# Performance work log

Measured on AMD Instinct MI355X. Metric: run time of the kernel, lower is better.

## Reference

```python
import jax, jax.numpy as jnp
import numpy as np

T, S, B, D, H, DH, DI = 1024, 1024, 4, 1024, 16, 64, 4096
SCALE = 1.0 / (DH ** 0.5)


def _ln(x, g, b, eps=1e-5):
    m = jnp.mean(x, axis=-1, keepdims=True)
    v = jnp.mean((x - m) ** 2, axis=-1, keepdims=True)
    return (x - m) * jax.lax.rsqrt(v + eps) * g + b


def setup_inputs() -> dict:
    key = jax.random.key(0)
    ks = jax.random.split(key, 16)
    s = 0.02
    inp = {
        "dec_inp": jax.random.normal(ks[0], (T, B, D), jnp.float32),
        "enc_out": jax.random.normal(ks[1], (T, B, D), jnp.float32),
        # causal mask for self-attn: [qlen, klen, bsz], True = masked
        "dec_mask": jnp.broadcast_to(jnp.triu(jnp.ones((T, T), bool), 1)[:, :, None], (T, T, B)),
        # encoder padding mask: [klen, bsz], last 128 positions padded
        "enc_mask": jnp.broadcast_to((jnp.arange(S) >= S - 128)[:, None], (S, B)),
        # self-attn params
        "W_q1": jax.random.normal(ks[2], (D, H * DH), jnp.float32) * s,
        "W_kv1": jax.random.normal(ks[3], (D, 2 * H * DH), jnp.float32) * s,
        "W_o1": jax.random.normal(ks[4], (H * DH, D), jnp.float32) * s,
        "g1": jnp.ones((D,), jnp.float32), "b1": jnp.zeros((D,), jnp.float32),
        # cross-attn params
        "W_q2": jax.random.normal(ks[5], (D, H * DH), jnp.float32) * s,
        "W_kv2": jax.random.normal(ks[6], (D, 2 * H * DH), jnp.float32) * s,
        "W_o2": jax.random.normal(ks[7], (H * DH, D), jnp.float32) * s,
        "g2": jnp.ones((D,), jnp.float32), "b2": jnp.zeros((D,), jnp.float32),
        # FFN params
        "W_ff1": jax.random.normal(ks[8], (D, DI), jnp.float32) * s,
        "b_ff1": jnp.zeros((DI,), jnp.float32),
        "W_ff2": jax.random.normal(ks[9], (DI, D), jnp.float32) * s,
        "b_ff2": jnp.zeros((D,), jnp.float32),
        "g3": jnp.ones((D,), jnp.float32), "b3": jnp.zeros((D,), jnp.float32),
    }
    return inp


def reference(dec_inp, enc_out, dec_mask, enc_mask,
              W_q1, W_kv1, W_o1, g1, b1,
              W_q2, W_kv2, W_o2, g2, b2,
              W_ff1, b_ff1, W_ff2, b_ff2, g3, b3):
    # ---- self-attention (MultiHeadAttn, pre_lnorm=True, mems=None) ----
    # NOTE: q is computed from the UN-normalized h; k,v from LN(c) — faithful to source.
    c = _ln(dec_inp, g1, b1)
    q = (dec_inp @ W_q1).reshape(T, B, H, DH)
    kv = (c @ W_kv1)
    k, v = jnp.split(kv, 2, axis=-1)
    k = k.reshape(T, B, H, DH)
    v = v.reshape(T, B, H, DH)
    score = jnp.einsum('ibnd,jbnd->ijbn', q, k) * SCALE  # [T,T,B,H]
    score = jnp.where(dec_mask[:, :, :, None], -jnp.inf, score)
    prob = jax.nn.softmax(score, axis=1)
    vec = jnp.einsum('ijbn,jbnd->ibnd', prob, v).reshape(T, B, H * DH)
    out1 = dec_inp + vec @ W_o1

    # ---- cross-attention (ContextMultiHeadAttn, pre_lnorm=True) ----
    # NOTE: residual uses the layer-normed h (source reassigns h = layer_norm(h)).
    h2 = _ln(out1, g2, b2)
    q2 = (h2 @ W_q2).reshape(T, B, H, DH)
    kv2 = enc_out @ W_kv2  # enc_out is NOT layer-normed in source
    k2, v2 = jnp.split(kv2, 2, axis=-1)
    k2 = k2.reshape(S, B, H, DH)
    v2 = v2.reshape(S, B, H, DH)
    score2 = jnp.einsum('ibnd,jbnd->ijbn', q2, k2) * SCALE  # [T,S,B,H]
    score2 = jnp.where(enc_mask[None, :, :, None], -10000.0, score2)
    prob2 = jax.nn.softmax(score2, axis=1)
    vec2 = jnp.einsum('ijbn,jbnd->ibnd', prob2, v2).reshape(T, B, H * DH)
    out2 = h2 + vec2 @ W_o2

    # ---- position-wise FFN (pre_lnorm) ----
    h3 = _ln(out2, g3, b3)
    core = jax.nn.gelu(h3 @ W_ff1 + b_ff1, approximate=False) @ W_ff2 + b_ff2
    return out2 + core
```

## Files before the change

kernel.cpp:

```cpp
#include <hip/hip_runtime.h>
#include <hip/hip_bf16.h>

#define T_ 1024
#define S_ 1024
#define B_ 4
#define D_ 1024
#define H_ 16
#define DH_ 64
#define DI_ 4096
#define NTOK 4096

typedef __attribute__((ext_vector_type(8))) short bf16x8;
typedef __attribute__((ext_vector_type(4))) float f32x4;

__device__ __forceinline__ short f2bf(float f) {
  unsigned u = __builtin_bit_cast(unsigned, f);
  u += 0x7fffu + ((u >> 16) & 1u);
  return (short)(u >> 16);
}

__device__ __forceinline__ void g2l16(const void* g, void* l) {
  __builtin_amdgcn_global_load_lds(
      (const __attribute__((address_space(1))) unsigned int*)g,
      (__attribute__((address_space(3))) unsigned int*)l, 16, 0, 0);
}

__device__ __forceinline__ void bar() {
  asm volatile("" ::: "memory");
  __builtin_amdgcn_s_barrier();
  asm volatile("" ::: "memory");
}

template <int EPI>
__global__ __launch_bounds__(512, 2) void gemm8p(
    const short* __restrict__ A, const short* __restrict__ Bt,
    float* __restrict__ outF, short* __restrict__ outB,
    const float* __restrict__ res, const float* __restrict__ bias,
    int M, int N, int K) {
  __shared__ short sA[2][256 * 64];
  __shared__ short sB[2][256 * 64];
  const int tid = threadIdx.x;
  const int lane = tid & 63;
  const int w = tid >> 6;
  const int wm = w >> 2, wn = w & 3;
  const int r15 = lane & 15, g4 = lane >> 4;
  const size_t row0 = (size_t)blockIdx.x * 256;
  const size_t col0 = (size_t)blockIdx.y * 256;

  f32x4 acc[8][4];
#pragma unroll
  for (int i = 0; i < 8; i++)
#pragma unroll
    for (int j = 0; j < 4; j++) acc[i][j] = (f32x4){0.f, 0.f, 0.f, 0.f};

  auto stageA = [&](int buf, int s, int kt) {
    const int k0 = kt << 6;
#pragma unroll
    for (int j = 0; j < 2; ++j) {
      const int c = j * 8 + w;
      const int rb = ((c >> 3) << 7) + (s << 6) + ((c & 7) << 3);
      const int row = rb + (lane >> 3);
      const int col = k0 + (((lane & 7) ^ (row & 7)) << 3);
      g2l16(A + (row0 + row) * (size_t)K + col, &sA[buf][rb * 64]);
    }
  };
  auto stageB = [&](int buf, int s, int kt) {
    const int k0 = kt << 6;
#pragma unroll
    for (int j = 0; j < 2; ++j) {
      const int c = j * 8 + w;
      const int rb = ((c >> 2) << 6) + (s << 5) + ((c & 3) << 3);
      const int row = rb + (lane >> 3);
      const int col = k0 + (((lane & 7) ^ (row & 7)) << 3);
      g2l16(Bt + (col0 + row) * (size_t)K + col, &sB[buf][rb * 64]);
    }
  };

  const int nk = K >> 6;
  stageA(0, 0, 0); stageA(0, 1, 0); stageB(0, 0, 0); stageB(0, 1, 0);
  if (nk > 1) {
    stageA(1, 0, 1); stageB(1, 1, 1);
    asm volatile("s_waitcnt vmcnt(4)" ::: "memory");
  } else {
    asm volatile("s_waitcnt vmcnt(0)" ::: "memory");
  }
  bar();

  bf16x8 af[4][2], bv0[2][2], bv1[2][2];
  for (int t = 0; t < nk; ++t) {
    const int cur = t & 1;
    const short* cA = sA[cur];
    const short* cB = sB[cur];
#pragma unroll
    for (int mi = 0; mi < 4; mi++) {
      const int rowA = wm * 128 + mi * 16 + r15;
#pragma unroll
      for (int kk = 0; kk < 2; kk++)
        af[mi][kk] = *(const bf16x8*)(cA + rowA * 64 +
                                      (((kk * 4 + g4) ^ (rowA & 7)) << 3));
    }
#pragma unroll
    for (int ni = 0; ni < 2; ni++) {
      const int rowB = wn * 64 + ni * 16 + r15;
#pragma unroll
      for (int kk = 0; kk < 2; kk++)
        bv0[ni][kk] = *(const bf16x8*)(cB + rowB * 64 +
                                       (((kk * 4 + g4) ^ (rowB & 7)) << 3));
    }
    if (t + 1 < nk) stageA(cur ^ 1, 1, t + 1);
    bar();
    asm volatile("s_waitcnt lgkmcnt(0)" ::: "memory");
    __builtin_amdgcn_s_setprio(1);
#pragma unroll
    for (int kk = 0; kk < 2; kk++)
#pragma unroll
      for (int mi = 0; mi < 4; mi++)
#pragma unroll
        for (int ni = 0; ni < 2; ni++)
          acc[mi][ni] = __builtin_amdgcn_mfma_f32_16x16x32_bf16(
              af[mi][kk], bv0[ni][kk], acc[mi][ni], 0, 0, 0);
    __builtin_amdgcn_s_setprio(0);
    bar();
#pragma unroll
    for (int ni = 0; ni < 2; ni++) {
      const int rowB = wn * 64 + (2 + ni) * 16 + r15;
#pragma unroll
      for (int kk = 0; kk < 2; kk++)
        bv1[ni][kk] = *(const bf16x8*)(cB + rowB * 64 +
                                       (((kk * 4 + g4) ^ (rowB & 7)) << 3));
    }
    if (t + 1 < nk) stageB(cur ^ 1, 0, t + 1);
    bar();
    asm volatile("s_waitcnt lgkmcnt(0)" ::: "memory");
    __builtin_amdgcn_s_setprio(1);
#pragma unroll
    for (int kk = 0; kk < 2; kk++)
#pragma unroll
      for (int mi = 0; mi < 4; mi++)
#pragma unroll
        for (int ni = 0; ni < 2; ni++)
          acc[mi][2 + ni] = __builtin_amdgcn_mfma_f32_16x16x32_bf16(
              af[mi][kk], bv1[ni][kk], acc[mi][2 + ni], 0, 0, 0);
    __builtin_amdgcn_s_setprio(0);
    bar();
#pragma unroll
    for (int mi = 0; mi < 4; mi++) {
      const int rowA = wm * 128 + (4 + mi) * 16 + r15;
#pragma unroll
      for (int kk = 0; kk < 2; kk++)
        af[mi][kk] = *(const bf16x8*)(cA + rowA * 64 +
                                      (((kk * 4 + g4) ^ (rowA & 7)) << 3));
    }
    if (t + 2 < nk) stageA(cur, 0, t + 2);
    bar();
    asm volatile("s_waitcnt lgkmcnt(0)" ::: "memory");
    __builtin_amdgcn_s_setprio(1);
#pragma unroll
    for (int kk = 0; kk < 2; kk++)
#pragma unroll
      for (int mi = 0; mi < 4; mi++)
#pragma unroll
        for (int ni = 0; ni < 2; ni++)
          acc[4 + mi][2 + ni] = __builtin_amdgcn_mfma_f32_16x16x32_bf16(
              af[mi][kk], bv1[ni][kk], acc[4 + mi][2 + ni], 0, 0, 0);
    __builtin_amdgcn_s_setprio(0);
    bar();
    if (t + 2 < nk) stageB(cur, 1, t + 2);
    bar();
    asm volatile("s_waitcnt lgkmcnt(0)" ::: "memory");
    __builtin_amdgcn_s_setprio(1);
#pragma unroll
    for (int kk = 0; kk < 2; kk++)
#pragma unroll
      for (int mi = 0; mi < 4; mi++)
#pragma unroll
        for (int ni = 0; ni < 2; ni++)
          acc[4 + mi][ni] = __builtin_amdgcn_mfma_f32_16x16x32_bf16(
              af[mi][kk], bv0[ni][kk], acc[4 + mi][ni], 0, 0, 0);
    __builtin_amdgcn_s_setprio(0);
    if (t + 2 < nk)
      asm volatile("s_waitcnt vmcnt(4)" ::: "memory");
    else if (t + 1 < nk)
      asm volatile("s_waitcnt vmcnt(0)" ::: "memory");
    bar();
  }

#pragma unroll
  for (int mi = 0; mi < 8; mi++) {
    size_t row = row0 + wm * 128 + mi * 16 + (g4 << 2);
#pragma unroll
    for (int ni = 0; ni < 4; ni++) {
      size_t col = col0 + wn * 64 + ni * 16 + r15;
      float bcol = (EPI == 2 || EPI == 3) ? bias[col] : 0.f;
#pragma unroll
      for (int r = 0; r < 4; r++) {
        size_t idx = (row + r) * (size_t)N + col;
        float v = acc[mi][ni][r];
        if (EPI == 0) {
          outB[idx] = f2bf(v);
        } else if (EPI == 1) {
          outF[idx] = v + res[idx];
        } else if (EPI == 2) {
          float x = v + bcol;
          float gl = 0.5f * x * (1.f + erff(x * 0.70710678118654752f));
          outB[idx] = f2bf(gl);
        } else {
          outF[idx] = v + bcol + res[idx];
        }
      }
    }
  }
}

template <int EPI, int BN>
__global__ __launch_bounds__(256, 2) void gemm_bt(
    const short* __restrict__ A, const short* __restrict__ Bt,
    float* __restrict__ outF, short* __restrict__ outB,
    const float* __restrict__ res, const float* __restrict__ bias,
    int M, int N, int K) {
  constexpr int WCOLS = BN / 64;
  constexpr int MI = (WCOLS == 2) ? 4 : 2;
  constexpr int BLOADS = BN / 32;
  __shared__ short sA[2][128 * 64];
  __shared__ short sB[2][BN * 64];
  const int tid = threadIdx.x;
  const int lane = tid & 63;
  const int w = tid >> 6;
  const int wr = (WCOLS == 2) ? (w >> 1) : w;
  const int wc = (WCOLS == 2) ? (w & 1) : 0;
  const int r15 = lane & 15, g4 = lane >> 4;
  const size_t row0 = (size_t)blockIdx.x * 128;
  const size_t col0 = (size_t)blockIdx.y * BN;

  f32x4 acc[MI][4];
#pragma unroll
  for (int i = 0; i < MI; i++)
#pragma unroll
    for (int j = 0; j < 4; j++) acc[i][j] = (f32x4){0.f, 0.f, 0.f, 0.f};

  auto stage = [&](int buf, int kt) {
    const int k0 = kt << 6;
#pragma unroll
    for (int i = 0; i < 4; i++) {
      int flat = i * 256 + tid;
      int row = flat >> 3;
      int col = k0 + (((flat & 7) ^ (row & 7)) << 3);
      g2l16(A + (row0 + row) * (size_t)K + col, &sA[buf][(i * 256 + w * 64) * 8]);
    }
#pragma unroll
    for (int i = 0; i < BLOADS; i++) {
      int flat = i * 256 + tid;
      int row = flat >> 3;
      int col = k0 + (((flat & 7) ^ (row & 7)) << 3);
      g2l16(Bt + (col0 + row) * (size_t)K + col, &sB[buf][(i * 256 + w * 64) * 8]);
    }
  };

  stage(0, 0);
  __syncthreads();

  const int nk = K >> 6;
  for (int kt = 0; kt < nk; ++kt) {
    const int cur = kt & 1;
    if (kt + 1 < nk) stage(cur ^ 1, kt + 1);
#pragma unroll
    for (int kk = 0; kk < 2; ++kk) {
      bf16x8 af[MI], bfr[4];
#pragma unroll
      for (int mi = 0; mi < MI; mi++) {
        int rowA = wr * (MI * 16) + mi * 16 + r15;
        af[mi] = *(const bf16x8*)(&sA[cur][rowA * 64 +
                                           (((kk * 4 + g4) ^ (rowA & 7)) << 3)]);
      }
#pragma unroll
      for (int ni = 0; ni < 4; ni++) {
        int rowB = wc * 64 + ni * 16 + r15;
        bfr[ni] = *(const bf16x8*)(&sB[cur][rowB * 64 +
                                            (((kk * 4 + g4) ^ (rowB & 7)) << 3)]);
      }
#pragma unroll
      for (int mi = 0; mi < MI; mi++)
#pragma unroll
        for (int ni = 0; ni < 4; ni++)
          acc[mi][ni] = __builtin_amdgcn_mfma_f32_16x16x32_bf16(af[mi], bfr[ni],
                                                                acc[mi][ni], 0, 0, 0);
    }
    __syncthreads();
  }

#pragma unroll
  for (int mi = 0; mi < MI; mi++) {
    size_t row = row0 + wr * (MI * 16) + mi * 16 + (g4 << 2);
#pragma unroll
    for (int ni = 0; ni < 4; ni++) {
      size_t col = col0 + wc * 64 + ni * 16 + r15;
      float bcol = (EPI == 2 || EPI == 3) ? bias[col] : 0.f;
#pragma unroll
      for (int r = 0; r < 4; r++) {
        size_t idx = (row + r) * (size_t)N + col;
        float v = acc[mi][ni][r];
        if (EPI == 0) {
          outB[idx] = f2bf(v);
        } else if (EPI == 1) {
          outF[idx] = v + res[idx];
        } else if (EPI == 2) {
          float x = v + bcol;
          float gl = 0.5f * x * (1.f + erff(x * 0.70710678118654752f));
          outB[idx] = f2bf(gl);
        } else {
          outF[idx] = v + bcol + res[idx];
        }
      }
    }
  }
}

__global__ __launch_bounds__(256, 2) void qkv_k(
    const short* __restrict__ Aq, const short* __restrict__ Bq,
    short* __restrict__ Qb,
    const short* __restrict__ Akv, const short* __restrict__ Bkv,
    short* __restrict__ Kgp, short* __restrict__ Vgp) {
  __shared__ short sA[2][128 * 64];
  __shared__ short sB[2][64 * 64];
  const int tid = threadIdx.x;
  const int lane = tid & 63;
  const int w = tid >> 6;
  const int r15 = lane & 15, g4 = lane >> 4;
  const bool isQ = blockIdx.y < 16;
  const short* __restrict__ A = isQ ? Aq : Akv;
  const short* __restrict__ Bt = isQ ? Bq : Bkv;
  const size_t row0 = (size_t)blockIdx.x * 128;
  const size_t col0 = (size_t)(isQ ? blockIdx.y : blockIdx.y - 16) * 64;
  const int K = 1024;

  f32x4 acc[2][4];
#pragma unroll
  for (int i = 0; i < 2; i++)
#pragma unroll
    for (int j = 0; j < 4; j++) acc[i][j] = (f32x4){0.f, 0.f, 0.f, 0.f};

  auto stage = [&](int buf, int kt) {
    const int k0 = kt << 6;
#pragma unroll
    for (int i = 0; i < 4; i++) {
      int flat = i * 256 + tid;
      int row = flat >> 3;
      int col = k0 + (((flat & 7) ^ (row & 7)) << 3);
      g2l16(A + (row0 + row) * (size_t)K + col, &sA[buf][(i * 256 + w * 64) * 8]);
    }
#pragma unroll
    for (int i = 0; i < 2; i++) {
      int flat = i * 256 + tid;
      int row = flat >> 3;
      int col = k0 + (((flat & 7) ^ (row & 7)) << 3);
      g2l16(Bt + (col0 + row) * (size_t)K + col, &sB[buf][(i * 256 + w * 64) * 8]);
    }
  };

  stage(0, 0);
  __syncthreads();

  const int nk = K >> 6;
  for (int kt = 0; kt < nk; ++kt) {
    const int cur = kt & 1;
    if (kt + 1 < nk) stage(cur ^ 1, kt + 1);
#pragma unroll
    for (int kk = 0; kk < 2; ++kk) {
      bf16x8 af[2], bfr[4];
#pragma unroll
      for (int mi = 0; mi < 2; mi++) {
        int rowA = w * 32 + mi * 16 + r15;
        af[mi] = *(const bf16x8*)(&sA[cur][rowA * 64 +
                                           (((kk * 4 + g4) ^ (rowA & 7)) << 3)]);
      }
#pragma unroll
      for (int ni = 0; ni < 4; ni++) {
        int rowB = ni * 16 + r15;
        bfr[ni] = *(const bf16x8*)(&sB[cur][rowB * 64 +
                                            (((kk * 4 + g4) ^ (rowB & 7)) << 3)]);
      }
#pragma unroll
      for (int mi = 0; mi < 2; mi++)
#pragma unroll
        for (int ni = 0; ni < 4; ni++)
          acc[mi][ni] = __builtin_amdgcn_mfma_f32_16x16x32_bf16(af[mi], bfr[ni],
                                                                acc[mi][ni], 0, 0, 0);
    }
    __syncthreads();
  }

#pragma unroll
  for (int mi = 0; mi < 2; mi++) {
    size_t row = row0 + w * 32 + mi * 16 + (g4 << 2);
#pragma unroll
    for (int ni = 0; ni < 4; ni++) {
      size_t col = col0 + ni * 16 + r15;
#pragma unroll
      for (int r = 0; r < 4; r++) {
        float v = acc[mi][ni][r];
        if (isQ) {
          Qb[(row + r) * 1024 + col] = f2bf(v);
        } else {
          int tt = (int)(row + r) >> 2;
          int bb = (int)(row + r) & 3;
          int cc = (int)col;
          if (cc < 1024) {
            int hh = cc >> 6, dd = cc & 63;
            size_t base = (size_t)(bb * 16 + hh) * 65536 + (size_t)tt * 64;
            Kgp[base + ((((dd >> 3) ^ (tt & 7)) << 3) | (dd & 7))] = f2bf(v * 0.125f);
          } else {
            int hh = (cc >> 6) - 16, dd = cc & 63;
            size_t base = (size_t)(bb * 16 + hh) * 65536 + (size_t)(tt >> 6) * 4096;
            Vgp[base + ((tt >> 3) & 7) * 512 + dd * 8 + (tt & 7)] = f2bf(v);
          }
        }
      }
    }
  }
}

template <int MODE>
__global__ __launch_bounds__(256, 2) void attn_k2(const short* __restrict__ Qm,
                                                  const short* __restrict__ Kg,
                                                  const short* __restrict__ Vg,
                                                  short* __restrict__ Om) {
  __shared__ short Kl[2][4096];
  __shared__ short Vl[2][4096];
  __shared__ short Pl[4][2048];
  const int tid = threadIdx.x;
  const int lane = tid & 63;
  const int w = tid >> 6;
  const int r15 = lane & 15, g4 = lane >> 4;
  const int bh = blockIdx.x;
  const int by = blockIdx.y;
  const int qt = (MODE == 0) ? ((by < 4) ? by : 11 - by) : by;
  const int b = bh >> 4, h = bh & 15;
  const int qbase = qt * 128 + w * 32;
  const int ktDiag = qbase >> 6;

  bf16x8 qf[2][2];
#pragma unroll
  for (int g = 0; g < 2; g++)
#pragma unroll
    for (int hf = 0; hf < 2; hf++) {
      int row = qbase + g * 16 + r15;
      qf[g][hf] = *(const bf16x8*)(Qm + ((size_t)(row * 4 + b)) * 1024 + h * 64 +
                                   hf * 32 + g4 * 8);
    }

  const size_t kvbase = (size_t)bh * 65536;
  const int nkt = (MODE == 0) ? (2 * qt + 2) : 14;

  f32x4 o[2][4];
#pragma unroll
  for (int g = 0; g < 2; g++)
#pragma unroll
    for (int ni = 0; ni < 4; ni++) o[g][ni] = (f32x4){0.f, 0.f, 0.f, 0.f};
  float mrun[2][4], lrun[2][4];
#pragma unroll
  for (int g = 0; g < 2; g++)
#pragma unroll
    for (int r = 0; r < 4; r++) { mrun[g][r] = -1e30f; lrun[g][r] = 0.f; }

  {
    const size_t tb = kvbase;
#pragma unroll
    for (int i = 0; i < 2; i++) {
      g2l16(Kg + tb + (size_t)(i * 256 + tid) * 8, &Kl[0][(i * 256 + w * 64) * 8]);
      g2l16(Vg + tb + (size_t)(i * 256 + tid) * 8, &Vl[0][(i * 256 + w * 64) * 8]);
    }
  }
  __syncthreads();

  for (int kt = 0; kt < nkt; kt++) {
    const int cur = kt & 1;
    if (kt + 1 < nkt) {
      const size_t tb = kvbase + (size_t)(kt + 1) * 4096;
#pragma unroll
      for (int i = 0; i < 2; i++) {
        g2l16(Kg + tb + (size_t)(i * 256 + tid) * 8,
              &Kl[cur ^ 1][(i * 256 + w * 64) * 8]);
        g2l16(Vg + tb + (size_t)(i * 256 + tid) * 8,
              &Vl[cur ^ 1][(i * 256 + w * 64) * 8]);
      }
    }

    const bool active = (MODE == 1) || (kt * 64 <= qbase + 31);
    if (active) {
      bf16x8 kb[4][2];
#pragma unroll
      for (int ni = 0; ni < 4; ni++) {
        int row = ni * 16 + r15;
        kb[ni][0] = *(const bf16x8*)(&Kl[cur][row * 64 + ((g4 ^ (row & 7)) << 3)]);
        kb[ni][1] =
            *(const bf16x8*)(&Kl[cur][row * 64 + (((g4 + 4) ^ (row & 7)) << 3)]);
      }
      f32x4 sf[2][4];
#pragma unroll
      for (int g = 0; g < 2; g++)
#pragma unroll
        for (int ni = 0; ni < 4; ni++) {
          f32x4 s = (f32x4){0.f, 0.f, 0.f, 0.f};
          s = __builtin_amdgcn_mfma_f32_16x16x32_bf16(qf[g][0], kb[ni][0], s, 0, 0, 0);
          s = __builtin_amdgcn_mfma_f32_16x16x32_bf16(qf[g][1], kb[ni][1], s, 0, 0, 0);
          sf[g][ni] = s;
        }
      if (MODE == 0 && kt >= ktDiag) {
#pragma unroll
        for (int g = 0; g < 2; g++)
#pragma unroll
          for (int ni = 0; ni < 4; ni++)
#pragma unroll
            for (int r = 0; r < 4; r++) {
              int q = qbase + g * 16 + g4 * 4 + r;
              int key = kt * 64 + ni * 16 + r15;
              if (key > q) sf[g][ni][r] = -1e30f;
            }
      }
#pragma unroll
      for (int g = 0; g < 2; g++) {
        float corr[4];
#pragma unroll
        for (int r = 0; r < 4; r++) {
          float m = fmaxf(fmaxf(sf[g][0][r], sf[g][1][r]),
                          fmaxf(sf[g][2][r], sf[g][3][r]));
          m = fmaxf(m, __shfl_xor(m, 1));
          m = fmaxf(m, __shfl_xor(m, 2));
          m = fmaxf(m, __shfl_xor(m, 4));
          m = fmaxf(m, __shfl_xor(m, 8));
          float mn = fmaxf(mrun[g][r], m);
          corr[r] = __expf(mrun[g][r] - mn);
          mrun[g][r] = mn;
        }
        float rs[4] = {0.f, 0.f, 0.f, 0.f};
#pragma unroll
        for (int ni = 0; ni < 4; ni++)
#pragma unroll
          for (int r = 0; r < 4; r++) {
            float p = __expf(sf[g][ni][r] - mrun[g][r]);
            sf[g][ni][r] = p;
            rs[r] += p;
          }
#pragma unroll
        for (int r = 0; r < 4; r++) {
          rs[r] += __shfl_xor(rs[r], 1);
          rs[r] += __shfl_xor(rs[r], 2);
          rs[r] += __shfl_xor(rs[r], 4);
          rs[r] += __shfl_xor(rs[r], 8);
          lrun[g][r] = lrun[g][r] * corr[r] + rs[r];
        }
#pragma unroll
        for (int ni = 0; ni < 4; ni++)
#pragma unroll
          for (int r = 0; r < 4; r++) o[g][ni][r] *= corr[r];
#pragma unroll
        for (int ni = 0; ni < 4; ni++)
#pragma unroll
          for (int r = 0; r < 4; r++) {
            int qr = g * 16 + g4 * 4 + r;
            int key = ni * 16 + r15;
            Pl[w][qr * 64 + ((((key >> 3) ^ ((qr >> 1) & 7)) << 3) | (key & 7))] =
                f2bf(sf[g][ni][r]);
          }
      }
#pragma unroll
      for (int kk = 0; kk < 2; kk++) {
        int gw = kk * 4 + g4;
        bf16x8 pa0 = *(const bf16x8*)(&Pl[w][r15 * 64 + ((gw ^ ((r15 >> 1) & 7)) << 3)]);
        bf16x8 pa1 =
            *(const bf16x8*)(&Pl[w][(16 + r15) * 64 + ((gw ^ ((r15 >> 1) & 7)) << 3)]);
#pragma unroll
        for (int ni = 0; ni < 4; ni++) {
          bf16x8 vb = *(const bf16x8*)(&Vl[cur][(gw * 64 + ni * 16 + r15) * 8]);
          o[0][ni] = __builtin_amdgcn_mfma_f32_16x16x32_bf16(pa0, vb, o[0][ni], 0, 0, 0);
          o[1][ni] = __builtin_amdgcn_mfma_f32_16x16x32_bf16(pa1, vb, o[1][ni], 0, 0, 0);
        }
      }
    }
    __syncthreads();
  }

#pragma unroll
  for (int g = 0; g < 2; g++) {
    float inv[4];
#pragma unroll
    for (int r = 0; r < 4; r++) inv[r] = 1.f / lrun[g][r];
#pragma unroll
    for (int ni = 0; ni < 4; ni++) {
      int col = h * 64 + ni * 16 + r15;
#pragma unroll
      for (int r = 0; r < 4; r++) {
        int tg = qbase + g * 16 + g4 * 4 + r;
        Om[((size_t)(tg * 4 + b)) * 1024 + col] = f2bf(o[g][ni][r] * inv[r]);
      }
    }
  }
}

__global__ __launch_bounds__(256) void ln_k(const float* __restrict__ x,
                                            const float* __restrict__ gw,
                                            const float* __restrict__ bw,
                                            float* __restrict__ outF,
                                            short* __restrict__ outB,
                                            short* __restrict__ outXB) {
  const int row = blockIdx.x, tid = threadIdx.x;
  const float4 v = ((const float4*)(x + (size_t)row * 1024))[tid];
  float s = v.x + v.y + v.z + v.w;
  float ss = v.x * v.x + v.y * v.y + v.z * v.z + v.w * v.w;
#pragma unroll
  for (int d = 32; d >= 1; d >>= 1) {
    s += __shfl_xor(s, d);
    ss += __shfl_xor(ss, d);
  }
  __shared__ float red[8];
  const int w = tid >> 6;
  if ((tid & 63) == 0) { red[w] = s; red[4 + w] = ss; }
  __syncthreads();
  s = red[0] + red[1] + red[2] + red[3];
  ss = red[4] + red[5] + red[6] + red[7];
  const float mean = s * (1.f / 1024.f);
  const float var = ss * (1.f / 1024.f) - mean * mean;
  const float rstd = rsqrtf(var + 1e-5f);
  const float4 gv = ((const float4*)gw)[tid];
  const float4 bv = ((const float4*)bw)[tid];
  float4 y;
  y.x = (v.x - mean) * rstd * gv.x + bv.x;
  y.y = (v.y - mean) * rstd * gv.y + bv.y;
  y.z = (v.z - mean) * rstd * gv.z + bv.z;
  y.w = (v.w - mean) * rstd * gv.w + bv.w;
  if (outF) ((float4*)(outF + (size_t)row * 1024))[tid] = y;
  if (outB) {
    short4 ob;
    ob.x = f2bf(y.x); ob.y = f2bf(y.y); ob.z = f2bf(y.z); ob.w = f2bf(y.w);
    ((short4*)(outB + (size_t)row * 1024))[tid] = ob;
  }
  if (outXB) {
    short4 ob;
    ob.x = f2bf(v.x); ob.y = f2bf(v.y); ob.z = f2bf(v.z); ob.w = f2bf(v.w);
    ((short4*)(outXB + (size_t)row * 1024))[tid] = ob;
  }
}

__global__ __launch_bounds__(256) void prep_k(
    const float* __restrict__ Wq1, const float* __restrict__ Wkv1,
    const float* __restrict__ Wo1, const float* __restrict__ Wq2,
    const float* __restrict__ Wkv2, const float* __restrict__ Wo2,
    const float* __restrict__ Wff1, const float* __restrict__ Wff2,
    const float* __restrict__ enc,
    short* __restrict__ q1t, short* __restrict__ kv1t, short* __restrict__ o1t,
    short* __restrict__ q2t, short* __restrict__ kv2t, short* __restrict__ o2t,
    short* __restrict__ ff1t, short* __restrict__ ff2t, short* __restrict__ ebf) {
  const int id = blockIdx.x;
  const int tid = threadIdx.x;
  if (id >= 4096) {
    const size_t i = (size_t)(id - 4096) * 256 + tid;
    const float4 v = ((const float4*)enc)[i];
    short4 ob;
    ob.x = f2bf(v.x); ob.y = f2bf(v.y); ob.z = f2bf(v.z); ob.w = f2bf(v.w);
    ((short4*)ebf)[i] = ob;
    return;
  }
  const float* in;
  short* out;
  int K, N, base;
  if (id < 256)       { in = Wq1;  out = q1t;  K = 1024; N = 1024; base = 0; }
  else if (id < 768)  { in = Wkv1; out = kv1t; K = 1024; N = 2048; base = 256; }
  else if (id < 1024) { in = Wo1;  out = o1t;  K = 1024; N = 1024; base = 768; }
  else if (id < 1280) { in = Wq2;  out = q2t;  K = 1024; N = 1024; base = 1024; }
  else if (id < 1792) { in = Wkv2; out = kv2t; K = 1024; N = 2048; base = 1280; }
  else if (id < 2048) { in = Wo2;  out = o2t;  K = 1024; N = 1024; base = 1792; }
  else if (id < 3072) { in = Wff1; out = ff1t; K = 1024; N = 4096; base = 2048; }
  else                { in = Wff2; out = ff2t; K = 4096; N = 1024; base = 3072; }
  const int lid = id - base;
  const int nkb = K >> 6;
  const int k0 = (lid % nkb) * 64;
  const int n0 = (lid / nkb) * 64;

  __shared__ float t[64][65];
#pragma unroll
  for (int i = 0; i < 16; i++) {
    int flat = i * 256 + tid;
    int r = flat >> 6, c = flat & 63;
    t[r][c] = in[(size_t)(k0 + r) * N + n0 + c];
  }
  __syncthreads();
#pragma unroll
  for (int i = 0; i < 16; i++) {
    int flat = i * 256 + tid;
    int r = flat >> 6, c = flat & 63;
    out[(size_t)(n0 + r) * K + k0 + c] = f2bf(t[c][r]);
  }
}

extern "C" void kernel_launch(void* const* d_in, const int* in_sizes, int n_in,
                              void* d_out, int out_size, void* d_ws, size_t ws_size,
                              hipStream_t stream) {
  const float* dec_inp = (const float*)d_in[0];
  const float* enc_out = (const float*)d_in[1];
  const float* W_q1 = (const float*)d_in[4];
  const float* W_kv1 = (const float*)d_in[5];
  const float* W_o1 = (const float*)d_in[6];
  const float* g1 = (const float*)d_in[7];
  const float* b1 = (const float*)d_in[8];
  const float* W_q2 = (const float*)d_in[9];
  const float* W_kv2 = (const float*)d_in[10];
  const float* W_o2 = (const float*)d_in[11];
  const float* g2 = (const float*)d_in[12];
  const float* b2 = (const float*)d_in[13];
  const float* W_ff1 = (const float*)d_in[14];
  const float* b_ff1 = (const float*)d_in[15];
  const float* W_ff2 = (const float*)d_in[16];
  const float* b_ff2 = (const float*)d_in[17];
  const float* g3 = (const float*)d_in[18];
  const float* b3 = (const float*)d_in[19];
  float* out = (float*)d_out;

  char* ws = (char*)d_ws;
  size_t off = 0;
  auto alloc = [&](size_t bytes) -> void* {
    void* p = ws + off;
    off += (bytes + 255) & ~(size_t)255;
    return p;
  };
  short* Wq1t = (short*)alloc(1024ull * 1024 * 2);
  short* Wkv1t = (short*)alloc(2048ull * 1024 * 2);
  short* Wo1t = (short*)alloc(1024ull * 1024 * 2);
  short* Wq2t = (short*)alloc(1024ull * 1024 * 2);
  short* Wkv2t = (short*)alloc(2048ull * 1024 * 2);
  short* Wo2t = (short*)alloc(1024ull * 1024 * 2);
  short* Wff1t = (short*)alloc(4096ull * 1024 * 2);
  short* Wff2t = (short*)alloc(1024ull * 4096 * 2);
  short* Xbf = (short*)alloc((size_t)NTOK * 1024 * 2);
  short* Ebf = (short*)alloc((size_t)NTOK * 1024 * 2);
  short* Cbf = (short*)alloc((size_t)NTOK * 1024 * 2);
  short* Qb = (short*)alloc((size_t)NTOK * 1024 * 2);
  short* Kg = (short*)alloc(64ull * 65536 * 2);
  short* Vg = (short*)alloc(64ull * 65536 * 2);
  short* VECb = (short*)alloc((size_t)NTOK * 1024 * 2);
  float* OUT1 = (float*)alloc((size_t)NTOK * 1024 * 4);
  float* H2f = (float*)alloc((size_t)NTOK * 1024 * 4);
  float* OUT2 = (float*)alloc((size_t)NTOK * 1024 * 4);
  short* FF1 = (short*)alloc((size_t)NTOK * 4096 * 2);
  short* H2b = Xbf;
  short* H3b = Cbf;

  dim3 blk(256, 1, 1);

  prep_k<<<8192, blk, 0, stream>>>(W_q1, W_kv1, W_o1, W_q2, W_kv2, W_o2, W_ff1,
                                   W_ff2, enc_out, Wq1t, Wkv1t, Wo1t, Wq2t,
                                   Wkv2t, Wo2t, Wff1t, Wff2t, Ebf);
  ln_k<<<4096, blk, 0, stream>>>(dec_inp, g1, b1, nullptr, Cbf, Xbf);

  qkv_k<<<dim3(32, 48), blk, 0, stream>>>(Xbf, Wq1t, Qb, Cbf, Wkv1t, Kg, Vg);
  attn_k2<0><<<dim3(64, 8), blk, 0, stream>>>(Qb, Kg, Vg, VECb);
  gemm_bt<1, 64><<<dim3(32, 16), blk, 0, stream>>>(
      VECb, Wo1t, OUT1, nullptr, dec_inp, nullptr, 4096, 1024, 1024);
  ln_k<<<4096, blk, 0, stream>>>(OUT1, g2, b2, H2f, H2b, nullptr);
  qkv_k<<<dim3(32, 48), blk, 0, stream>>>(H2b, Wq2t, Qb, Ebf, Wkv2t, Kg, Vg);
  attn_k2<1><<<dim3(64, 8), blk, 0, stream>>>(Qb, Kg, Vg, VECb);
  gemm_bt<1, 64><<<dim3(32, 16), blk, 0, stream>>>(
      VECb, Wo2t, OUT2, nullptr, H2f, nullptr, 4096, 1024, 1024);
  ln_k<<<4096, blk, 0, stream>>>(OUT2, g3, b3, nullptr, H3b, nullptr);
  gemm8p<2><<<dim3(16, 16), dim3(512, 1, 1), 0, stream>>>(
      H3b, Wff1t, nullptr, FF1, nullptr, b_ff1, 4096, 4096, 1024);
  gemm_bt<3, 64><<<dim3(32, 16), blk, 0, stream>>>(
      FF1, Wff2t, out, nullptr, OUT2, b_ff2, 4096, 1024, 4096);
}
```

Before: 351.2 us.

## Split-K the FFN down-projection GEMM with a separate reduction kernel

```diff
diff --git a/kernel.cpp b/kernel.cpp
--- a/kernel.cpp
+++ b/kernel.cpp
@@ -217,7 +217,7 @@
     const short* __restrict__ A, const short* __restrict__ Bt,
     float* __restrict__ outF, short* __restrict__ outB,
     const float* __restrict__ res, const float* __restrict__ bias,
-    int M, int N, int K) {
+    int M, int N, int Kst, int Kloop) {
   constexpr int WCOLS = BN / 64;
   constexpr int MI = (WCOLS == 2) ? 4 : 2;
   constexpr int BLOADS = BN / 32;
@@ -231,6 +231,8 @@
   const int r15 = lane & 15, g4 = lane >> 4;
   const size_t row0 = (size_t)blockIdx.x * 128;
   const size_t col0 = (size_t)blockIdx.y * BN;
+  const int kOff = (EPI == 5) ? blockIdx.z * Kloop : 0;
+  float* outP = (EPI == 5) ? outF + (size_t)blockIdx.z * M * (size_t)N : outF;
 
   f32x4 acc[MI][4];
 #pragma unroll
@@ -239,27 +241,27 @@
     for (int j = 0; j < 4; j++) acc[i][j] = (f32x4){0.f, 0.f, 0.f, 0.f};
 
   auto stage = [&](int buf, int kt) {
-    const int k0 = kt << 6;
+    const int k0 = kOff + (kt << 6);
 #pragma unroll
     for (int i = 0; i < 4; i++) {
       int flat = i * 256 + tid;
       int row = flat >> 3;
       int col = k0 + (((flat & 7) ^ (row & 7)) << 3);
-      g2l16(A + (row0 + row) * (size_t)K + col, &sA[buf][(i * 256 + w * 64) * 8]);
+      g2l16(A + (row0 + row) * (size_t)Kst + col, &sA[buf][(i * 256 + w * 64) * 8]);
     }
 #pragma unroll
     for (int i = 0; i < BLOADS; i++) {
       int flat = i * 256 + tid;
       int row = flat >> 3;
       int col = k0 + (((flat & 7) ^ (row & 7)) << 3);
-      g2l16(Bt + (col0 + row) * (size_t)K + col, &sB[buf][(i * 256 + w * 64) * 8]);
+      g2l16(Bt + (col0 + row) * (size_t)Kst + col, &sB[buf][(i * 256 + w * 64) * 8]);
     }
   };
 
   stage(0, 0);
   __syncthreads();
 
-  const int nk = K >> 6;
+  const int nk = Kloop >> 6;
   for (int kt = 0; kt < nk; ++kt) {
     const int cur = kt & 1;
     if (kt + 1 < nk) stage(cur ^ 1, kt + 1);
@@ -294,25 +296,38 @@
 #pragma unroll
     for (int ni = 0; ni < 4; ni++) {
       size_t col = col0 + wc * 64 + ni * 16 + r15;
-      float bcol = (EPI == 2 || EPI == 3) ? bias[col] : 0.f;
 #pragma unroll
       for (int r = 0; r < 4; r++) {
         size_t idx = (row + r) * (size_t)N + col;
         float v = acc[mi][ni][r];
-        if (EPI == 0) {
-          outB[idx] = f2bf(v);
-        } else if (EPI == 1) {
+        if (EPI == 1) {
           outF[idx] = v + res[idx];
-        } else if (EPI == 2) {
-          float x = v + bcol;
-          float gl = 0.5f * x * (1.f + erff(x * 0.70710678118654752f));
-          outB[idx] = f2bf(gl);
+        } else if (EPI == 5) {
+          outP[idx] = v;
         } else {
-          outF[idx] = v + bcol + res[idx];
+          outF[idx] = v + res[idx];
         }
       }
     }
   }
+}
+
+__global__ __launch_bounds__(256) void ffn2_fin(const float* __restrict__ P,
+                                                const float* __restrict__ res,
+                                                const float* __restrict__ bias,
+                                                float* __restrict__ out) {
+  const int row = blockIdx.x, tid = threadIdx.x;
+  const size_t i = (size_t)row * 256 + tid;
+  const float4 p0 = ((const float4*)P)[i];
+  const float4 p1 = ((const float4*)P)[i + (size_t)NTOK * 256];
+  const float4 rv = ((const float4*)res)[i];
+  const float4 bv = ((const float4*)bias)[tid];
+  float4 y;
+  y.x = p0.x + p1.x + rv.x + bv.x;
+  y.y = p0.y + p1.y + rv.y + bv.y;
+  y.z = p0.z + p1.z + rv.z + bv.z;
+  y.w = p0.w + p1.w + rv.w + bv.w;
+  ((float4*)out)[i] = y;
 }
 
 __global__ __launch_bounds__(256, 2) void qkv_k(
@@ -743,6 +758,7 @@
   short* FF1 = (short*)alloc((size_t)NTOK * 4096 * 2);
   short* H2b = Xbf;
   short* H3b = Cbf;
+  float* PartF = (float*)Qb;
 
   dim3 blk(256, 1, 1);
 
@@ -754,15 +770,16 @@
   qkv_k<<<dim3(32, 48), blk, 0, stream>>>(Xbf, Wq1t, Qb, Cbf, Wkv1t, Kg, Vg);
   attn_k2<0><<<dim3(64, 8), blk, 0, stream>>>(Qb, Kg, Vg, VECb);
   gemm_bt<1, 64><<<dim3(32, 16), blk, 0, stream>>>(
-      VECb, Wo1t, OUT1, nullptr, dec_inp, nullptr, 4096, 1024, 1024);
+      VECb, Wo1t, OUT1, nullptr, dec_inp, nullptr, 4096, 1024, 1024, 1024);
   ln_k<<<4096, blk, 0, stream>>>(OUT1, g2, b2, H2f, H2b, nullptr);
   qkv_k<<<dim3(32, 48), blk, 0, stream>>>(H2b, Wq2t, Qb, Ebf, Wkv2t, Kg, Vg);
   attn_k2<1><<<dim3(64, 8), blk, 0, stream>>>(Qb, Kg, Vg, VECb);
   gemm_bt<1, 64><<<dim3(32, 16), blk, 0, stream>>>(
-      VECb, Wo2t, OUT2, nullptr, H2f, nullptr, 4096, 1024, 1024);
+      VECb, Wo2t, OUT2, nullptr, H2f, nullptr, 4096, 1024, 1024, 1024);
   ln_k<<<4096, blk, 0, stream>>>(OUT2, g3, b3, nullptr, H3b, nullptr);
   gemm8p<2><<<dim3(16, 16), dim3(512, 1, 1), 0, stream>>>(
       H3b, Wff1t, nullptr, FF1, nullptr, b_ff1, 4096, 4096, 1024);
-  gemm_bt<3, 64><<<dim3(32, 16), blk, 0, stream>>>(
-      FF1, Wff2t, out, nullptr, OUT2, b_ff2, 4096, 1024, 4096);
-}
+  gemm_bt<5, 64><<<dim3(32, 16, 2), blk, 0, stream>>>(
+      FF1, Wff2t, PartF, nullptr, nullptr, nullptr, 4096, 1024, 4096, 2048);
+  ffn2_fin<<<4096, blk, 0, stream>>>(PartF, OUT2, b_ff2, out);
+}
```

New measurement: 364.6 us. 3.8% more time.
